# Optimization experiments

Hardware: AMD Instinct MI355X
Metric: run time of the kernel (lower is better)

The kernel has to match this reference:

```python
import jax, jax.numpy as jnp
import numpy as np

V = 16          # polygon vertices
MAXN = 4 * V    # padded buffer for clipped polygon


def _safe(d):
    return jnp.where(d == 0, jnp.ones_like(d), d)


def _is_inside(p1, p2, q):
    # cross product test; R <= 0 means inside (clockwise convention). q: [M,2]
    R = (p2[0] - p1[0]) * (q[..., 1] - p1[1]) - (p2[1] - p1[1]) * (q[..., 0] - p1[0])
    return R <= 0


def _intersection(p1, p2, p3, p4):
    # line (p1,p2) x line (p3,p4); p1,p2: [M,2] subject edges, p3,p4: [2] clip edge
    dx12 = p2[..., 0] - p1[..., 0]
    dy12 = p2[..., 1] - p1[..., 1]
    dx34 = p4[0] - p3[0]
    m1 = dy12 / _safe(dx12)
    b1 = p1[..., 1] - m1 * p1[..., 0]
    m2 = (p4[1] - p3[1]) / _safe(dx34)
    b2 = p3[1] - m2 * p3[0]
    x_gen = (b2 - b1) / _safe(m1 - m2)
    y_gen = m1 * x_gen + b1
    # subject edge vertical
    x_v1 = p1[..., 0]
    y_v1 = m2 * x_v1 + b2
    # clip edge vertical
    x_v2 = jnp.full_like(x_gen, p3[0])
    y_v2 = m1 * x_v2 + b1
    vert1 = dx12 == 0
    vert2 = dx34 == 0
    x = jnp.where(vert1, x_v1, jnp.where(vert2, x_v2, x_gen))
    y = jnp.where(vert1, y_v1, jnp.where(vert2, y_v2, y_gen))
    return jnp.stack([x, y], axis=-1)


def _clip_edge(carry, edge):
    # one Sutherland-Hodgman pass: clip padded polygon (poly, n) by half-plane (c1,c2)
    poly, n = carry
    c1, c2 = edge
    idx = jnp.arange(MAXN)
    valid = idx < n
    nsafe = jnp.maximum(n, 1)
    prev = poly[(idx - 1) % nsafe]
    cur = poly
    ins_c = _is_inside(c1, c2, cur)
    ins_p = _is_inside(c1, c2, prev)
    inter = _intersection(prev, cur, c1, c2)
    emit_i = valid & (ins_c ^ ins_p)   # emit intersection on crossing
    emit_c = valid & ins_c             # emit current vertex when inside
    cnt = emit_i.astype(jnp.int32) + emit_c.astype(jnp.int32)
    off = jnp.cumsum(cnt) - cnt        # exclusive prefix sum of emit counts
    DUMP = MAXN                        # extra slot for suppressed writes
    ii = jnp.where(emit_i, jnp.minimum(off, DUMP), DUMP)
    ic = jnp.where(emit_c, jnp.minimum(off + emit_i.astype(jnp.int32), DUMP), DUMP)
    buf = jnp.zeros((MAXN + 1, 2), poly.dtype)
    buf = buf.at[ii].set(inter)
    buf = buf.at[ic].set(cur)
    new_n = jnp.minimum(off[-1] + cnt[-1], MAXN)
    return (buf[:MAXN], new_n), None


def _clip(subject, clip_poly):
    poly = jnp.zeros((MAXN, 2), subject.dtype).at[:V].set(subject)
    n = jnp.int32(V)
    c1s = jnp.roll(clip_poly, 1, axis=0)  # edge (v[i-1], v[i]) as in reference
    (poly, n), _ = jax.lax.scan(_clip_edge, (poly, n), (c1s, clip_poly))
    return poly, n


def _area_padded(poly, n):
    # faithful to original area(): shoelace with vertex-0/1 term double counted
    idx = jnp.arange(poly.shape[0])
    valid = (idx < n).astype(poly.dtype)
    nsafe = jnp.maximum(n, 1)
    nxt = (idx + 1) % nsafe
    x, y = poly[:, 0], poly[:, 1]
    left = jnp.sum(valid * x * y[nxt])
    right = jnp.sum(valid * y * x[nxt])
    i1 = 1 % nsafe
    has = (n > 0).astype(poly.dtype)
    left = left + has * x[0] * y[i1]
    right = right + has * y[0] * x[i1]
    return jnp.abs(0.5 * (right - left))


def _iou(pred_poly, tgt_poly):
    cp, n = _clip(pred_poly, tgt_poly)
    a_i = _area_padded(cp, n)
    a_p = _area_padded(pred_poly, jnp.int32(V))
    a_g = _area_padded(tgt_poly, jnp.int32(V))
    inter = jnp.where(a_i == 0.0, jnp.minimum(a_p, a_g), jnp.zeros_like(a_i)) + a_i
    union = a_g + a_p - inter
    return inter / (union + 1e-6)


def setup_inputs() -> dict:
    key = jax.random.key(0)
    k1, k2, k3 = jax.random.split(key, 3)
    B, K, H, W = 16, 128, 256, 256
    output = jax.random.normal(k1, (B, 2 * V, H, W), dtype=jnp.float32)
    target = jax.random.normal(k2, (B, K, 2 * V), dtype=jnp.float32)
    mask = jnp.ones((B, K), dtype=jnp.float32)
    ind = jax.random.randint(k3, (B, K), 0, H * W, dtype=jnp.int32)
    return {"output": output, "mask": mask, "ind": ind, "target": target}


def reference(output, mask, ind, target):
    B, C, H, W = output.shape
    K = ind.shape[1]
    # _transpose_and_gather_feat: [B,C,H,W] -> [B,HW,C] -> gather at ind -> [B,K,C]
    feat = output.reshape(B, C, H * W).transpose(0, 2, 1)
    pred = jnp.take_along_axis(feat, ind[:, :, None], axis=1)
    pred_poly = pred.reshape(B * K, V, 2)
    tgt_poly = target.reshape(B * K, V, 2)
    ious = jax.vmap(_iou)(pred_poly, tgt_poly)
    loss_iou = jnp.sum(ious * mask.reshape(-1))
    loss = 1.0 - loss_iou / (mask.sum() + 1e-6)
    return loss
```

## Files before the change

kernel.cpp:

```cpp
#include <hip/hip_runtime.h>

#define V 16
#define MAXN 64
#define WAVES_PER_BLOCK 4

__device__ __forceinline__ float safe_(float d) { return (d == 0.0f) ? 1.0f : d; }

__device__ __forceinline__ int lower_popcount(unsigned long long m) {
    return __builtin_amdgcn_mbcnt_hi((unsigned)(m >> 32),
           __builtin_amdgcn_mbcnt_lo((unsigned)m, 0));
}

__global__ __launch_bounds__(256) void poly_iou_kernel(
    const float* __restrict__ output,
    const float* __restrict__ mask,
    const int*   __restrict__ ind,
    const float* __restrict__ target,
    float* __restrict__ iou_ws,
    int BK, int K, int HW)
{
    __shared__ float bufx[WAVES_PER_BLOCK][MAXN];
    __shared__ float bufy[WAVES_PER_BLOCK][MAXN];

    const int lane = threadIdx.x & 63;
    const int wave = threadIdx.x >> 6;
    int pair = blockIdx.x * WAVES_PER_BLOCK + wave;
    const bool live = pair < BK;
    if (!live) pair = 0;
    const int b = pair / K;

    float px = 0.0f, py = 0.0f;
    float sx = 0.0f, sy = 0.0f;
    float cx = 0.0f, cy = 0.0f;
    if (lane < V) {
        const int idx = ind[pair];
        const float* ob = output + ((size_t)b * (2 * V)) * (size_t)HW;
        sx = ob[(size_t)(2 * lane) * HW + idx];
        sy = ob[(size_t)(2 * lane + 1) * HW + idx];
        const float2 t2 = ((const float2*)(target + (size_t)pair * (2 * V)))[lane];
        cx = t2.x;
        cy = t2.y;
        px = sx; py = sy;
    }
    int n = V;

    for (int t = 0; t < V; ++t) {
        if (n == 0) break;

        const int t1 = (t + V - 1) & (V - 1);
        const float c1x = __shfl(cx, t1), c1y = __shfl(cy, t1);
        const float c2x = __shfl(cx, t),  c2y = __shfl(cy, t);

        const int pidx = (lane == 0) ? (n - 1) : (lane - 1);
        const float prx = __shfl(px, pidx);
        const float pry = __shfl(py, pidx);

        const float Rc = (c2x - c1x) * (py - c1y) - (c2y - c1y) * (px - c1x);
        const int ins_c = (Rc <= 0.0f) ? 1 : 0;
        const int ins_p = __shfl(ins_c, pidx);

        const bool valid  = (lane < n);
        const bool emit_i = valid && ((ins_c ^ ins_p) != 0);
        const bool emit_c = valid && (ins_c != 0);

        const float dx12 = px - prx, dy12 = py - pry;
        const float dx34 = c2x - c1x;
        const float m1 = dy12 / safe_(dx12);
        const float b1 = pry - m1 * prx;
        const float m2 = (c2y - c1y) / safe_(dx34);
        const float b2 = c1y - m2 * c1x;
        const float xg = (b2 - b1) / safe_(m1 - m2);
        const float yg = m1 * xg + b1;
        float ix, iy;
        if (dx12 == 0.0f)      { ix = prx; iy = m2 * prx + b2; }
        else if (dx34 == 0.0f) { ix = c1x; iy = m1 * c1x + b1; }
        else                   { ix = xg;  iy = yg; }

        const unsigned long long bi = __ballot(emit_i ? 1 : 0);
        const unsigned long long bc = __ballot(emit_c ? 1 : 0);
        const int off   = lower_popcount(bi) + lower_popcount(bc);
        const int total = __popcll(bi) + __popcll(bc);

        if (emit_i) {
            const int p0 = off;
            if (p0 < MAXN) { bufx[wave][p0] = ix; bufy[wave][p0] = iy; }
        }
        if (emit_c) {
            const int p1 = off + (emit_i ? 1 : 0);
            if (p1 < MAXN) { bufx[wave][p1] = px; bufy[wave][p1] = py; }
        }

        n = (total < MAXN) ? total : MAXN;
        px = (lane < n) ? bufx[wave][lane] : 0.0f;
        py = (lane < n) ? bufy[wave][lane] : 0.0f;
    }

    auto area = [&](float x, float y, int nn) -> float {
        const int ns = (nn > 0) ? nn : 1;
        const int nxt = (lane + 1 == ns) ? 0 : (lane + 1);
        const float xn = __shfl(x, nxt);
        const float yn = __shfl(y, nxt);
        const bool val = (lane < nn);
        float l = val ? x * yn : 0.0f;
        float r = val ? y * xn : 0.0f;
        #pragma unroll
        for (int o = 32; o > 0; o >>= 1) {
            l += __shfl_xor(l, o);
            r += __shfl_xor(r, o);
        }
        const int i1 = (ns > 1) ? 1 : 0;
        const float x0 = __shfl(x, 0),  y0 = __shfl(y, 0);
        const float xi = __shfl(x, i1), yi = __shfl(y, i1);
        if (nn > 0) { l += x0 * yi; r += y0 * xi; }
        return fabsf(0.5f * (r - l));
    };

    const float a_i = area(px, py, n);
    const float a_p = area(sx, sy, V);
    const float a_g = area(cx, cy, V);

    const float inter = ((a_i == 0.0f) ? fminf(a_p, a_g) : 0.0f) + a_i;
    const float uni   = a_g + a_p - inter;
    const float iou   = inter / (uni + 1e-6f);

    if (live && lane == 0) {
        iou_ws[pair] = iou * mask[pair];
    }
}

__global__ __launch_bounds__(256) void poly_finalize_kernel(
    const float* __restrict__ iou_ws,
    const float* __restrict__ mask,
    float* __restrict__ out, int BK)
{
    float si = 0.0f, sm = 0.0f;
    for (int i = threadIdx.x; i < BK; i += 256) {
        si += iou_ws[i];
        sm += mask[i];
    }
    #pragma unroll
    for (int o = 32; o > 0; o >>= 1) {
        si += __shfl_xor(si, o);
        sm += __shfl_xor(sm, o);
    }
    __shared__ float a[4], c[4];
    const int wave = threadIdx.x >> 6;
    if ((threadIdx.x & 63) == 0) { a[wave] = si; c[wave] = sm; }
    __syncthreads();
    if (threadIdx.x == 0) {
        const float ti = a[0] + a[1] + a[2] + a[3];
        const float tm = c[0] + c[1] + c[2] + c[3];
        out[0] = 1.0f - ti / (tm + 1e-6f);
    }
}

extern "C" void kernel_launch(void* const* d_in, const int* in_sizes, int n_in,
                              void* d_out, int out_size, void* d_ws, size_t ws_size,
                              hipStream_t stream) {
    const float* output = (const float*)d_in[0];
    const float* mask   = (const float*)d_in[1];
    const int*   ind    = (const int*)d_in[2];
    const float* target = (const float*)d_in[3];
    float* out = (float*)d_out;
    float* iou_ws = (float*)d_ws;

    const int BK = in_sizes[1];
    const int B  = 16;
    const int K  = BK / B;
    const int HW = in_sizes[0] / (B * 2 * V);

    const int grid = (BK + WAVES_PER_BLOCK - 1) / WAVES_PER_BLOCK;
    poly_iou_kernel<<<grid, 64 * WAVES_PER_BLOCK, 0, stream>>>(
        output, mask, ind, target, iou_ws, BK, K, HW);
    poly_finalize_kernel<<<1, 256, 0, stream>>>(iou_ws, mask, out, BK);
}
```

Measured before the change: 174.3 us.

## Fuse finalize into IoU kernel via last-block counter and skip non-crossing clip passes

Merges the single-block reduction into the main IoU kernel: each block bumps an atomic counter and the last block to finish performs the final sum, removing the second launch. A memset of the counter is added to the stream. Inside the clipping loop, the previous-vertex inside test is recomputed locally instead of shuffled, and passes with no edge crossings skip the intersection math and shared-memory rewrite (or exit early when all vertices are outside). Per-wave scalar values (pair index, ind, mask) are made uniform with readfirstlane so they load once.

```diff
diff --git a/kernel.cpp b/kernel.cpp
--- a/kernel.cpp
+++ b/kernel.cpp
@@ -11,33 +11,40 @@
            __builtin_amdgcn_mbcnt_lo((unsigned)m, 0));
 }
 
-__global__ __launch_bounds__(256) void poly_iou_kernel(
+__global__ __launch_bounds__(256) void poly_iou_fused_kernel(
     const float* __restrict__ output,
     const float* __restrict__ mask,
     const int*   __restrict__ ind,
     const float* __restrict__ target,
-    float* __restrict__ iou_ws,
-    int BK, int K, int HW)
+    unsigned int* __restrict__ counter,
+    float* __restrict__ iou_res,
+    float* __restrict__ out,
+    int BK, int K, int HW, int nblocks)
 {
     __shared__ float bufx[WAVES_PER_BLOCK][MAXN];
     __shared__ float bufy[WAVES_PER_BLOCK][MAXN];
+    __shared__ float red_a[WAVES_PER_BLOCK], red_c[WAVES_PER_BLOCK];
+    __shared__ int   last_flag;
 
     const int lane = threadIdx.x & 63;
     const int wave = threadIdx.x >> 6;
     int pair = blockIdx.x * WAVES_PER_BLOCK + wave;
     const bool live = pair < BK;
     if (!live) pair = 0;
-    const int b = pair / K;
+    const int pu = __builtin_amdgcn_readfirstlane(pair);
+    const int b  = pu / K;
+
+    const int   idx  = ind[pu];
+    const float mval = mask[pu];
 
     float px = 0.0f, py = 0.0f;
     float sx = 0.0f, sy = 0.0f;
     float cx = 0.0f, cy = 0.0f;
     if (lane < V) {
-        const int idx = ind[pair];
         const float* ob = output + ((size_t)b * (2 * V)) * (size_t)HW;
         sx = ob[(size_t)(2 * lane) * HW + idx];
         sy = ob[(size_t)(2 * lane + 1) * HW + idx];
-        const float2 t2 = ((const float2*)(target + (size_t)pair * (2 * V)))[lane];
+        const float2 t2 = ((const float2*)(target + (size_t)pu * (2 * V)))[lane];
         cx = t2.x;
         cy = t2.y;
         px = sx; py = sy;
@@ -55,13 +62,25 @@
         const float prx = __shfl(px, pidx);
         const float pry = __shfl(py, pidx);
 
-        const float Rc = (c2x - c1x) * (py - c1y) - (c2y - c1y) * (px - c1x);
-        const int ins_c = (Rc <= 0.0f) ? 1 : 0;
-        const int ins_p = __shfl(ins_c, pidx);
+        const float Rc = (c2x - c1x) * (py  - c1y) - (c2y - c1y) * (px  - c1x);
+        const float Rp = (c2x - c1x) * (pry - c1y) - (c2y - c1y) * (prx - c1x);
+        const bool ins_c = (Rc <= 0.0f);
+        const bool ins_p = (Rp <= 0.0f);
 
         const bool valid  = (lane < n);
-        const bool emit_i = valid && ((ins_c ^ ins_p) != 0);
-        const bool emit_c = valid && (ins_c != 0);
+        const bool emit_i = valid && (ins_c != ins_p);
+        const bool emit_c = valid && ins_c;
+
+        const unsigned long long bi = __ballot(emit_i ? 1 : 0);
+        const unsigned long long bc = __ballot(emit_c ? 1 : 0);
+
+        if (bi == 0ULL) {
+            if (bc == 0ULL) { n = 0; break; }
+            continue;
+        }
+
+        const int off   = lower_popcount(bi) + lower_popcount(bc);
+        const int total = __popcll(bi) + __popcll(bc);
 
         const float dx12 = px - prx, dy12 = py - pry;
         const float dx34 = c2x - c1x;
@@ -75,11 +94,6 @@
         if (dx12 == 0.0f)      { ix = prx; iy = m2 * prx + b2; }
         else if (dx34 == 0.0f) { ix = c1x; iy = m1 * c1x + b1; }
         else                   { ix = xg;  iy = yg; }
-
-        const unsigned long long bi = __ballot(emit_i ? 1 : 0);
-        const unsigned long long bc = __ballot(emit_c ? 1 : 0);
-        const int off   = lower_popcount(bi) + lower_popcount(bc);
-        const int total = __popcll(bi) + __popcll(bc);
 
         if (emit_i) {
             const int p0 = off;
@@ -124,18 +138,24 @@
     const float iou   = inter / (uni + 1e-6f);
 
     if (live && lane == 0) {
-        iou_ws[pair] = iou * mask[pair];
+        __hip_atomic_store(&iou_res[pu], iou * mval,
+                           __ATOMIC_RELEASE, __HIP_MEMORY_SCOPE_AGENT);
     }
-}
 
-__global__ __launch_bounds__(256) void poly_finalize_kernel(
-    const float* __restrict__ iou_ws,
-    const float* __restrict__ mask,
-    float* __restrict__ out, int BK)
-{
+    __syncthreads();
+    if (threadIdx.x == 0) {
+        const unsigned int old = __hip_atomic_fetch_add(
+            counter, 1u, __ATOMIC_ACQ_REL, __HIP_MEMORY_SCOPE_AGENT);
+        last_flag = (old == (unsigned)(nblocks - 1)) ? 1 : 0;
+    }
+    __syncthreads();
+    if (last_flag == 0) return;
+
+    __threadfence();
+
     float si = 0.0f, sm = 0.0f;
     for (int i = threadIdx.x; i < BK; i += 256) {
-        si += iou_ws[i];
+        si += __hip_atomic_load(&iou_res[i], __ATOMIC_RELAXED, __HIP_MEMORY_SCOPE_AGENT);
         sm += mask[i];
     }
     #pragma unroll
@@ -143,13 +163,11 @@
         si += __shfl_xor(si, o);
         sm += __shfl_xor(sm, o);
     }
-    __shared__ float a[4], c[4];
-    const int wave = threadIdx.x >> 6;
-    if ((threadIdx.x & 63) == 0) { a[wave] = si; c[wave] = sm; }
+    if (lane == 0) { red_a[wave] = si; red_c[wave] = sm; }
     __syncthreads();
     if (threadIdx.x == 0) {
-        const float ti = a[0] + a[1] + a[2] + a[3];
-        const float tm = c[0] + c[1] + c[2] + c[3];
+        const float ti = red_a[0] + red_a[1] + red_a[2] + red_a[3];
+        const float tm = red_c[0] + red_c[1] + red_c[2] + red_c[3];
         out[0] = 1.0f - ti / (tm + 1e-6f);
     }
 }
@@ -161,8 +179,6 @@
     const float* mask   = (const float*)d_in[1];
     const int*   ind    = (const int*)d_in[2];
     const float* target = (const float*)d_in[3];
-    float* out = (float*)d_out;
-    float* iou_ws = (float*)d_ws;
 
     const int BK = in_sizes[1];
     const int B  = 16;
@@ -170,7 +186,13 @@
     const int HW = in_sizes[0] / (B * 2 * V);
 
     const int grid = (BK + WAVES_PER_BLOCK - 1) / WAVES_PER_BLOCK;
-    poly_iou_kernel<<<grid, 64 * WAVES_PER_BLOCK, 0, stream>>>(
-        output, mask, ind, target, iou_ws, BK, K, HW);
-    poly_finalize_kernel<<<1, 256, 0, stream>>>(iou_ws, mask, out, BK);
+
+    unsigned int* counter = (unsigned int*)d_ws;
+    float* iou_res = (float*)((char*)d_ws + 256);
+
+    hipMemsetAsync(d_ws, 0, 4, stream);
+
+    poly_iou_fused_kernel<<<grid, 64 * WAVES_PER_BLOCK, 0, stream>>>(
+        output, mask, ind, target, counter, iou_res, (float*)d_out,
+        BK, K, HW, grid);
 }
```

Result: slower. 197.0 us (+13.0%).
